# Kernel tuning notes

Hardware: AMD Instinct MI355X
Metric: run time of the kernel (lower is better)

Reference implementation:

```python
import jax, jax.numpy as jnp
import numpy as np

B, N_NODES, N_EDGES = 2, 40962, 327680
ND, ED, HD, L = 256, 64, 512, 16  # node_dim, edge_dim, hidden_dim, n_layers
LN_EPS = 1e-5


def _ln(x, g, b):
    m = jnp.mean(x, axis=-1, keepdims=True)
    v = jnp.var(x, axis=-1, keepdims=True)
    return (x - m) * jax.lax.rsqrt(v + LN_EPS) * g + b


def setup_inputs() -> dict:
    key = jax.random.key(0)
    ks = jax.random.split(key, 8)
    def w(k, shape, fan_in):
        return jax.random.normal(k, shape, jnp.float32) * (1.0 / np.sqrt(fan_in))
    node_features = jax.random.normal(ks[0], (B, N_NODES, ND), jnp.float32)
    edge_features = jax.random.normal(ks[1], (N_EDGES, ED), jnp.float32)
    edge_index = jax.random.randint(ks[2], (2, N_EDGES), 0, N_NODES, dtype=jnp.int32)
    ein, nin = ED + 2 * ND, ND + ED
    return {
        "node_features": node_features,
        "edge_features": edge_features,
        "We1": w(ks[3], (L, ein, HD), ein), "be1": jnp.zeros((L, HD), jnp.float32),
        "We2": w(ks[4], (L, HD, ED), HD),   "be2": jnp.zeros((L, ED), jnp.float32),
        "ge": jnp.ones((L, ED), jnp.float32), "ble": jnp.zeros((L, ED), jnp.float32),
        "Wn1": w(ks[5], (L, nin, HD), nin), "bn1": jnp.zeros((L, HD), jnp.float32),
        "Wn2": w(ks[6], (L, HD, ND), HD),   "bn2": jnp.zeros((L, ND), jnp.float32),
        "gn": jnp.ones((L, ND), jnp.float32), "bln": jnp.zeros((L, ND), jnp.float32),
        "edge_index": edge_index,
    }


def reference(node_features, edge_features, We1, be1, We2, be2, ge, ble,
              Wn1, bn1, Wn2, bn2, gn, bln, edge_index):
    src, dst = edge_index[0], edge_index[1]
    n = node_features.shape[-2]
    stacked = (We1, be1, We2, be2, ge, ble, Wn1, bn1, Wn2, bn2, gn, bln)

    def single(x0):  # x0: (N, ND) — original loops over batch; we vmap
        def layer(carry, p):
            x, e = carry
            we1, b1, we2, b2, g_e, b_e, wn1, nb1, wn2, nb2, g_n, b_n = p
            # edge update: gather endpoints, MLP, residual
            m = jnp.concatenate([e, x[src], x[dst]], axis=-1)   # (E, ED+2*ND)
            h = jax.nn.silu(m @ we1 + b1)                        # (E, HD)
            e = e + _ln(h @ we2 + b2, g_e, b_e)                  # (E, ED)
            # node update: scatter-sum messages to destinations, MLP, residual
            agg = jax.ops.segment_sum(e, dst, num_segments=n)    # (N, ED)
            h = jax.nn.silu(jnp.concatenate([x, agg], axis=-1) @ wn1 + nb1)
            x = x + _ln(h @ wn2 + nb2, g_n, b_n)                 # (N, ND)
            return (x, e), None
        (x, _e), _ = jax.lax.scan(layer, (x0, edge_features), stacked)
        return x

    return jax.vmap(single)(node_features)
```

## Files before the change

### kernel.cpp

```cpp
#include <hip/hip_runtime.h>
#include <hip/hip_bf16.h>

#define N_NODES 40962
#define N_EDGES 327680
#define NDIM 256
#define EDIM 64
#define HDIM 512
#define NLAYERS 16

using bf16_t = __bf16;
using bf16x4 = __bf16 __attribute__((ext_vector_type(4)));
using bf16x8 = __bf16 __attribute__((ext_vector_type(8)));
using f32x4  = float __attribute__((ext_vector_type(4)));

__device__ __forceinline__ int clamp_idx(int v) {
    return v < 0 ? 0 : (v >= N_NODES ? N_NODES - 1 : v);
}

__device__ __forceinline__ bf16x8 zero8() {
    bf16x8 z;
#pragma unroll
    for (int j = 0; j < 8; ++j) z[j] = (bf16_t)0.f;
    return z;
}

__global__ void repack_w(const float* __restrict__ src, bf16_t* __restrict__ dst,
                         int K, int N, int tilesPer) {
    int idx = blockIdx.x * 256 + threadIdx.x;
    int lane = idx & 63;
    int t = idx >> 6;
    int l = t / tilesPer;
    int tile = t % tilesPer;
    if (l >= NLAYERS) return;
    int ntN = N >> 4;
    int k0 = (tile / ntN) << 5;
    int n0 = (tile % ntN) << 4;
    int k = k0 + (lane >> 4) * 8;
    int n = n0 + (lane & 15);
    const float* s = src + (size_t)l * K * N + (size_t)k * N + n;
    bf16x8 v;
#pragma unroll
    for (int j = 0; j < 8; ++j) v[j] = (bf16_t)s[(size_t)j * N];
    *(bf16x8*)(dst + (size_t)idx * 8) = v;
}

__global__ void init_e2(const float* __restrict__ ef, bf16_t* __restrict__ es, int n8) {
    const size_t per = (size_t)N_EDGES * EDIM;
    for (int i = blockIdx.x * 256 + threadIdx.x; i < n8; i += gridDim.x * 256) {
        float4 a = *(const float4*)(ef + (size_t)i * 8);
        float4 b = *(const float4*)(ef + (size_t)i * 8 + 4);
        bf16x8 v;
        v[0] = (bf16_t)a.x; v[1] = (bf16_t)a.y; v[2] = (bf16_t)a.z; v[3] = (bf16_t)a.w;
        v[4] = (bf16_t)b.x; v[5] = (bf16_t)b.y; v[6] = (bf16_t)b.z; v[7] = (bf16_t)b.w;
        *(bf16x8*)(es + (size_t)i * 8) = v;
        *(bf16x8*)(es + per + (size_t)i * 8) = v;
    }
}

__global__ void f32_to_bf16(const float* __restrict__ src, bf16_t* __restrict__ dst, int n8) {
    for (int i = blockIdx.x * 256 + threadIdx.x; i < n8; i += gridDim.x * 256) {
        float4 a = *(const float4*)(src + (size_t)i * 8);
        float4 b = *(const float4*)(src + (size_t)i * 8 + 4);
        bf16x8 v;
        v[0] = (bf16_t)a.x; v[1] = (bf16_t)a.y; v[2] = (bf16_t)a.z; v[3] = (bf16_t)a.w;
        v[4] = (bf16_t)b.x; v[5] = (bf16_t)b.y; v[6] = (bf16_t)b.z; v[7] = (bf16_t)b.w;
        *(bf16x8*)(dst + (size_t)i * 8) = v;
    }
}

__global__ void zero_f32(float* __restrict__ p, int n4) {
    float4 z; z.x = z.y = z.z = z.w = 0.f;
    for (int i = blockIdx.x * 256 + threadIdx.x; i < n4; i += gridDim.x * 256)
        *(float4*)(p + (size_t)i * 4) = z;
}

__global__ void hist_k(const int* __restrict__ eidx, int* __restrict__ deg) {
    int e = blockIdx.x * 256 + threadIdx.x;
    if (e < N_EDGES) atomicAdd(&deg[clamp_idx(eidx[N_EDGES + e])], 1);
}

__global__ void scan_k(const int* __restrict__ deg, int* __restrict__ off,
                       int* __restrict__ cur) {
    __shared__ int part[1024];
    const int t = threadIdx.x;
    const int C = (N_NODES + 1023) / 1024;
    int lo = t * C, hi = min((t + 1) * C, N_NODES);
    int s = 0;
    for (int i = lo; i < hi; ++i) s += deg[i];
    part[t] = s;
    __syncthreads();
    for (int d = 1; d < 1024; d <<= 1) {
        int v = (t >= d) ? part[t - d] : 0;
        __syncthreads();
        part[t] += v;
        __syncthreads();
    }
    int base = (t == 0) ? 0 : part[t - 1];
    for (int i = lo; i < hi; ++i) {
        off[i] = base;
        cur[i] = base;
        base += deg[i];
    }
    if (t == 1023) off[N_NODES] = part[1023];
}

__global__ void fill_k(const int* __restrict__ eidx, int* __restrict__ cur,
                       int* __restrict__ csr) {
    int e = blockIdx.x * 256 + threadIdx.x;
    if (e < N_EDGES) {
        int d = clamp_idx(eidx[N_EDGES + e]);
        int pos = atomicAdd(&cur[d], 1);
        csr[pos] = e;
    }
}

__global__ __launch_bounds__(512, 4)
void edge_kernel(const bf16_t* __restrict__ x16, bf16_t* __restrict__ es,
                 const int* __restrict__ eidx,
                 const bf16_t* __restrict__ w1p, const float* __restrict__ b1,
                 const bf16_t* __restrict__ w2p, const float* __restrict__ b2,
                 const float* __restrict__ gw, const float* __restrict__ bw) {
    __shared__ bf16_t smem[64 * 584];
    __shared__ int sSrc[64], sDst[64];
    float* red = (float*)(smem + 64 * 520);

    const int b   = blockIdx.y;
    const int e0  = blockIdx.x * 64;
    const int tid = threadIdx.x;

    const bf16_t* xb = x16 + (size_t)b * N_NODES * NDIM;
    bf16_t* eb = es + (size_t)b * N_EDGES * EDIM;

    if (tid < 64) {
        sSrc[tid] = clamp_idx(eidx[e0 + tid]);
        sDst[tid] = clamp_idx(eidx[N_EDGES + e0 + tid]);
    }
    __syncthreads();

    {
        int r = tid >> 3, c = (tid & 7) << 3;
        *(bf16x8*)&smem[r * 584 + c] = *(const bf16x8*)(eb + (size_t)(e0 + r) * EDIM + c);
    }
#pragma unroll
    for (int k = 0; k < 4; ++k) {
        int i = tid + k * 512;
        int r = i >> 5, c = (i & 31) << 3;
        *(bf16x8*)&smem[r * 584 + 64 + c] = *(const bf16x8*)(xb + (size_t)sSrc[r] * NDIM + c);
    }
#pragma unroll
    for (int k = 0; k < 4; ++k) {
        int i = tid + k * 512;
        int r = i >> 5, c = (i & 31) << 3;
        *(bf16x8*)&smem[r * 584 + 320 + c] = *(const bf16x8*)(xb + (size_t)sDst[r] * NDIM + c);
    }
    __syncthreads();

    const int wv = tid >> 6, lane = tid & 63;
    const int m16 = lane & 15, quad = lane >> 4;

    float bias1[4];
#pragma unroll
    for (int nt = 0; nt < 4; ++nt) bias1[nt] = b1[wv * 64 + nt * 16 + m16];

    f32x4 acc1[4][4];
#pragma unroll
    for (int mt = 0; mt < 4; ++mt)
#pragma unroll
        for (int nt = 0; nt < 4; ++nt) acc1[mt][nt] = (f32x4){0.f, 0.f, 0.f, 0.f};

    const bf16x8* W1 = (const bf16x8*)w1p;
#pragma unroll 2
    for (int kc = 0; kc < 18; ++kc) {
        bf16x8 af[4];
#pragma unroll
        for (int mt = 0; mt < 4; ++mt)
            af[mt] = *(const bf16x8*)&smem[(mt * 16 + m16) * 584 + kc * 32 + quad * 8];
        bf16x8 bfr[4];
#pragma unroll
        for (int nt = 0; nt < 4; ++nt)
            bfr[nt] = W1[(size_t)(kc * 32 + wv * 4 + nt) * 64 + lane];
#pragma unroll
        for (int mt = 0; mt < 4; ++mt)
#pragma unroll
            for (int nt = 0; nt < 4; ++nt)
                acc1[mt][nt] = __builtin_amdgcn_mfma_f32_16x16x32_bf16(af[mt], bfr[nt], acc1[mt][nt], 0, 0, 0);
    }
    __syncthreads();

#pragma unroll
    for (int mt = 0; mt < 4; ++mt)
#pragma unroll
        for (int nt = 0; nt < 4; ++nt)
#pragma unroll
            for (int r = 0; r < 4; ++r) {
                int row = mt * 16 + quad * 4 + r;
                int col = wv * 64 + nt * 16 + m16;
                float v = acc1[mt][nt][r] + bias1[nt];
                v = v / (1.f + __expf(-v));
                smem[row * 520 + col] = (bf16_t)v;
            }
    __syncthreads();

    const int strip = wv >> 1, nh = wv & 1;
    f32x4 acc2[2];
#pragma unroll
    for (int nt = 0; nt < 2; ++nt) acc2[nt] = (f32x4){0.f, 0.f, 0.f, 0.f};
    const bf16x8* W2 = (const bf16x8*)w2p;
#pragma unroll 2
    for (int kc = 0; kc < 16; ++kc) {
        bf16x8 a2 = *(const bf16x8*)&smem[(strip * 16 + m16) * 520 + kc * 32 + quad * 8];
#pragma unroll
        for (int nt = 0; nt < 2; ++nt) {
            bf16x8 b2f = W2[(size_t)(kc * 4 + nh * 2 + nt) * 64 + lane];
            acc2[nt] = __builtin_amdgcn_mfma_f32_16x16x32_bf16(a2, b2f, acc2[nt], 0, 0, 0);
        }
    }

    float bias2[2], g2[2], bl2[2];
#pragma unroll
    for (int nt = 0; nt < 2; ++nt) {
        int c = nh * 32 + nt * 16 + m16;
        bias2[nt] = b2[c];
        g2[nt]    = gw[c];
        bl2[nt]   = bw[c];
    }
    float v[4][2];
#pragma unroll
    for (int r = 0; r < 4; ++r) {
        float s1 = 0.f, s2 = 0.f;
#pragma unroll
        for (int nt = 0; nt < 2; ++nt) {
            v[r][nt] = acc2[nt][r] + bias2[nt];
            s1 += v[r][nt]; s2 += v[r][nt] * v[r][nt];
        }
#pragma unroll
        for (int off = 1; off < 16; off <<= 1) {
            s1 += __shfl_xor(s1, off);
            s2 += __shfl_xor(s2, off);
        }
        if (m16 == 0) {
            int row = strip * 16 + quad * 4 + r;
            red[row * 4 + nh * 2 + 0] = s1;
            red[row * 4 + nh * 2 + 1] = s2;
        }
    }
    __syncthreads();

#pragma unroll
    for (int r = 0; r < 4; ++r) {
        int row = strip * 16 + quad * 4 + r;
        float s1 = red[row * 4 + 0] + red[row * 4 + 2];
        float s2 = red[row * 4 + 1] + red[row * 4 + 3];
        float mean = s1 * (1.f / 64.f);
        float var  = s2 * (1.f / 64.f) - mean * mean;
        float rstd = rsqrtf(fmaxf(var, 0.f) + 1e-5f);
        int eid = e0 + row;
        const bf16_t* ebr = eb + (size_t)eid * EDIM;
#pragma unroll
        for (int nt = 0; nt < 2; ++nt) {
            int c = nh * 32 + nt * 16 + m16;
            float ln = (v[r][nt] - mean) * rstd * g2[nt] + bl2[nt];
            float en = (float)ebr[c] + ln;
            smem[row * 64 + c] = (bf16_t)en;
        }
    }
    __syncthreads();
    {
        int r = tid >> 3, c = (tid & 7) << 3;
        *(bf16x8*)(eb + (size_t)(e0 + r) * EDIM + c) = *(bf16x8*)&smem[r * 64 + c];
    }
}

__global__ __launch_bounds__(512, 4)
void node_kernel(float* __restrict__ xs, bf16_t* __restrict__ x16,
                 const bf16_t* __restrict__ es,
                 const int* __restrict__ off, const int* __restrict__ csr,
                 const bf16_t* __restrict__ w1p, const float* __restrict__ b1,
                 const bf16_t* __restrict__ w2p, const float* __restrict__ b2,
                 const float* __restrict__ gw, const float* __restrict__ bw) {
    __shared__ bf16_t smem[64 * 528];
    float* red = (float*)(smem + 64 * 520);

    const int b   = blockIdx.y;
    const int n0  = blockIdx.x * 64;
    const int tid = threadIdx.x;

    float* xb = xs + (size_t)b * N_NODES * NDIM;
    bf16_t* xhb = x16 + (size_t)b * N_NODES * NDIM;
    const bf16_t* eb = es + (size_t)b * N_EDGES * EDIM;

    const int wv = tid >> 6, lane = tid & 63;
    const int m16 = lane & 15, quad = lane >> 4;

#pragma unroll
    for (int k = 0; k < 4; ++k) {
        int i = tid + k * 512;
        int r = i >> 5, c = (i & 31) << 3;
        int node = n0 + r;
        bf16x8 v = (node < N_NODES) ? *(const bf16x8*)(xhb + (size_t)node * NDIM + c)
                                    : zero8();
        *(bf16x8*)&smem[r * 328 + c] = v;
    }
#pragma unroll 1
    for (int rr = 0; rr < 8; ++rr) {
        int row = wv * 8 + rr;
        int node = n0 + row;
        float acc = 0.f;
        if (node < N_NODES) {
            int js = off[node], je = off[node + 1];
            for (int j = js; j < je; ++j) {
                int eid = csr[j];
                acc += (float)eb[(size_t)eid * EDIM + lane];
            }
        }
        smem[row * 328 + 256 + lane] = (bf16_t)acc;
    }
    __syncthreads();

    float bias1[4];
#pragma unroll
    for (int nt = 0; nt < 4; ++nt) bias1[nt] = b1[wv * 64 + nt * 16 + m16];

    f32x4 acc1[4][4];
#pragma unroll
    for (int mt = 0; mt < 4; ++mt)
#pragma unroll
        for (int nt = 0; nt < 4; ++nt) acc1[mt][nt] = (f32x4){0.f, 0.f, 0.f, 0.f};

    const bf16x8* W1 = (const bf16x8*)w1p;
#pragma unroll 2
    for (int kc = 0; kc < 10; ++kc) {
        bf16x8 af[4];
#pragma unroll
        for (int mt = 0; mt < 4; ++mt)
            af[mt] = *(const bf16x8*)&smem[(mt * 16 + m16) * 328 + kc * 32 + quad * 8];
        bf16x8 bfr[4];
#pragma unroll
        for (int nt = 0; nt < 4; ++nt)
            bfr[nt] = W1[(size_t)(kc * 32 + wv * 4 + nt) * 64 + lane];
#pragma unroll
        for (int mt = 0; mt < 4; ++mt)
#pragma unroll
            for (int nt = 0; nt < 4; ++nt)
                acc1[mt][nt] = __builtin_amdgcn_mfma_f32_16x16x32_bf16(af[mt], bfr[nt], acc1[mt][nt], 0, 0, 0);
    }
    __syncthreads();

#pragma unroll
    for (int mt = 0; mt < 4; ++mt)
#pragma unroll
        for (int nt = 0; nt < 4; ++nt)
#pragma unroll
            for (int r = 0; r < 4; ++r) {
                int row = mt * 16 + quad * 4 + r;
                int col = wv * 64 + nt * 16 + m16;
                float v = acc1[mt][nt][r] + bias1[nt];
                v = v / (1.f + __expf(-v));
                smem[row * 520 + col] = (bf16_t)v;
            }
    __syncthreads();

    const int strip = wv >> 1, nh = wv & 1;
    f32x4 acc2[8];
#pragma unroll
    for (int nt = 0; nt < 8; ++nt) acc2[nt] = (f32x4){0.f, 0.f, 0.f, 0.f};
    const bf16x8* W2 = (const bf16x8*)w2p;
#pragma unroll 2
    for (int kc = 0; kc < 16; ++kc) {
        bf16x8 a2 = *(const bf16x8*)&smem[(strip * 16 + m16) * 520 + kc * 32 + quad * 8];
#pragma unroll
        for (int nt = 0; nt < 8; ++nt) {
            bf16x8 b2f = W2[(size_t)(kc * 16 + nh * 8 + nt) * 64 + lane];
            acc2[nt] = __builtin_amdgcn_mfma_f32_16x16x32_bf16(a2, b2f, acc2[nt], 0, 0, 0);
        }
    }

    float bias2[8], g8[8], bl8[8];
#pragma unroll
    for (int nt = 0; nt < 8; ++nt) {
        int c = nh * 128 + nt * 16 + m16;
        bias2[nt] = b2[c];
        g8[nt]    = gw[c];
        bl8[nt]   = bw[c];
    }
    float v[4][8];
#pragma unroll
    for (int r = 0; r < 4; ++r) {
        float s1 = 0.f, s2 = 0.f;
#pragma unroll
        for (int nt = 0; nt < 8; ++nt) {
            v[r][nt] = acc2[nt][r] + bias2[nt];
            s1 += v[r][nt]; s2 += v[r][nt] * v[r][nt];
        }
#pragma unroll
        for (int off2 = 1; off2 < 16; off2 <<= 1) {
            s1 += __shfl_xor(s1, off2);
            s2 += __shfl_xor(s2, off2);
        }
        if (m16 == 0) {
            int row = strip * 16 + quad * 4 + r;
            red[row * 4 + nh * 2 + 0] = s1;
            red[row * 4 + nh * 2 + 1] = s2;
        }
    }
    __syncthreads();

#pragma unroll
    for (int r = 0; r < 4; ++r) {
        int row = strip * 16 + quad * 4 + r;
        int node = n0 + row;
        if (node >= N_NODES) continue;
        float s1 = red[row * 4 + 0] + red[row * 4 + 2];
        float s2 = red[row * 4 + 1] + red[row * 4 + 3];
        float mean = s1 * (1.f / 256.f);
        float var  = s2 * (1.f / 256.f) - mean * mean;
        float rstd = rsqrtf(fmaxf(var, 0.f) + 1e-5f);
#pragma unroll
        for (int nt = 0; nt < 8; ++nt) {
            int c = nh * 128 + nt * 16 + m16;
            float ln = (v[r][nt] - mean) * rstd * g8[nt] + bl8[nt];
            float* px = &xb[(size_t)node * NDIM + c];
            float nv = *px + ln;
            *px = nv;
            xhb[(size_t)node * NDIM + c] = (bf16_t)nv;
        }
    }
}

extern "C" void kernel_launch(void* const* d_in, const int* in_sizes, int n_in,
                              void* d_out, int out_size, void* d_ws, size_t ws_size,
                              hipStream_t stream) {
    const float* nf   = (const float*)d_in[0];
    const float* ef   = (const float*)d_in[1];
    const float* We1  = (const float*)d_in[2];
    const float* be1  = (const float*)d_in[3];
    const float* We2  = (const float*)d_in[4];
    const float* be2  = (const float*)d_in[5];
    const float* ge   = (const float*)d_in[6];
    const float* ble  = (const float*)d_in[7];
    const float* Wn1  = (const float*)d_in[8];
    const float* bn1  = (const float*)d_in[9];
    const float* Wn2  = (const float*)d_in[10];
    const float* bn2  = (const float*)d_in[11];
    const float* gn   = (const float*)d_in[12];
    const float* bln  = (const float*)d_in[13];
    const int* eidx   = (const int*)d_in[14];

    float* xs = (float*)d_out;

    char* p = (char*)d_ws;
    bf16_t* es  = (bf16_t*)p; p += (size_t)2 * N_EDGES * EDIM * 2;
    bf16_t* x16 = (bf16_t*)p; p += (size_t)2 * N_NODES * NDIM * 2;
    bf16_t* w1ep = (bf16_t*)p; p += (size_t)NLAYERS * 576 * 512 * 2;
    bf16_t* w2ep = (bf16_t*)p; p += (size_t)NLAYERS * 512 * 64 * 2;
    bf16_t* w1np = (bf16_t*)p; p += (size_t)NLAYERS * 320 * 512 * 2;
    bf16_t* w2np = (bf16_t*)p; p += (size_t)NLAYERS * 512 * 256 * 2;
    int* deg = (int*)p; p += (size_t)40964 * 4;
    int* off = (int*)p; p += (size_t)40964 * 4;
    int* cur = (int*)p; p += (size_t)40964 * 4;
    int* csr = (int*)p; p += (size_t)N_EDGES * 4;

    repack_w<<<2304, 256, 0, stream>>>(We1, w1ep, 576, 512, 576);
    repack_w<<<256,  256, 0, stream>>>(We2, w2ep, 512, 64,  64);
    repack_w<<<1280, 256, 0, stream>>>(Wn1, w1np, 320, 512, 320);
    repack_w<<<1024, 256, 0, stream>>>(Wn2, w2np, 512, 256, 256);

    hipMemcpyAsync(xs, nf, (size_t)out_size * 4, hipMemcpyDeviceToDevice, stream);
    f32_to_bf16<<<2048, 256, 0, stream>>>(nf, x16, 2 * N_NODES * NDIM / 8);
    init_e2<<<2048, 256, 0, stream>>>(ef, es, N_EDGES * EDIM / 8);

    zero_f32<<<64, 256, 0, stream>>>((float*)deg, 40964 / 4);
    hist_k<<<N_EDGES / 256, 256, 0, stream>>>(eidx, deg);
    scan_k<<<1, 1024, 0, stream>>>(deg, off, cur);
    fill_k<<<N_EDGES / 256, 256, 0, stream>>>(eidx, cur, csr);

    for (int l = 0; l < NLAYERS; ++l) {
        edge_kernel<<<dim3(N_EDGES / 64, 2), 512, 0, stream>>>(
            x16, es, eidx,
            w1ep + (size_t)l * 576 * 512, be1 + l * 512,
            w2ep + (size_t)l * 512 * 64,  be2 + l * 64,
            ge + l * 64, ble + l * 64);
        node_kernel<<<dim3((N_NODES + 63) / 64, 2), 512, 0, stream>>>(
            xs, x16, es, off, csr,
            w1np + (size_t)l * 320 * 512, bn1 + l * 512,
            w2np + (size_t)l * 512 * 256, bn2 + l * 256,
            gn + l * 256, bln + l * 256);
    }
}
```

Before: 12.49 ms.

## Merge both batches into one 1024-thread block sharing weight fragments

Each edge and node block now handles the same 64 edges or nodes for both batch items, 128 rows in all, with 1024 threads. Every weight fragment loaded from global memory therefore feeds twice as many MFMAs, and the src/dst indices are shared across batches. LDS rows are XOR-swizzled instead of padded, with the edge input reordered (x_src, x_dst, e) to match. Biases are folded into the accumulator init and the node gather loop is unrolled by four. The larger blocks use more LDS and registers per block and may lower occupancy, and 1024-thread blocks with launch_bounds(1024,4) may spill.

```diff
diff --git a/kernel.cpp b/kernel.cpp
--- a/kernel.cpp
+++ b/kernel.cpp
@@ -13,6 +13,9 @@
 using bf16x8 = __bf16 __attribute__((ext_vector_type(8)));
 using f32x4  = float __attribute__((ext_vector_type(4)));
 
+#define SWE(r, eo) ((r) * 576 + ((eo) ^ (((r) & 7) << 3)))
+#define SWN(r, eo) ((r) * 512 + ((eo) ^ (((r) & 7) << 3)))
+
 __device__ __forceinline__ int clamp_idx(int v) {
     return v < 0 ? 0 : (v >= N_NODES ? N_NODES - 1 : v);
 }
@@ -25,7 +28,7 @@
 }
 
 __global__ void repack_w(const float* __restrict__ src, bf16_t* __restrict__ dst,
-                         int K, int N, int tilesPer) {
+                         int K, int N, int tilesPer, int mode) {
     int idx = blockIdx.x * 256 + threadIdx.x;
     int lane = idx & 63;
     int t = idx >> 6;
@@ -37,6 +40,7 @@
     int n0 = (tile % ntN) << 4;
     int k = k0 + (lane >> 4) * 8;
     int n = n0 + (lane & 15);
+    if (mode == 1) k = (k < 512) ? k + 64 : k - 512;
     const float* s = src + (size_t)l * K * N + (size_t)k * N + n;
     bf16x8 v;
 #pragma unroll
@@ -114,22 +118,20 @@
     }
 }
 
-__global__ __launch_bounds__(512, 4)
+__global__ __launch_bounds__(1024, 4)
 void edge_kernel(const bf16_t* __restrict__ x16, bf16_t* __restrict__ es,
                  const int* __restrict__ eidx,
                  const bf16_t* __restrict__ w1p, const float* __restrict__ b1,
                  const bf16_t* __restrict__ w2p, const float* __restrict__ b2,
                  const float* __restrict__ gw, const float* __restrict__ bw) {
-    __shared__ bf16_t smem[64 * 584];
+    __shared__ bf16_t smem[128 * 576];
+    __shared__ float red[128 * 4];
     __shared__ int sSrc[64], sDst[64];
-    float* red = (float*)(smem + 64 * 520);
-
-    const int b   = blockIdx.y;
+
     const int e0  = blockIdx.x * 64;
     const int tid = threadIdx.x;
-
-    const bf16_t* xb = x16 + (size_t)b * N_NODES * NDIM;
-    bf16_t* eb = es + (size_t)b * N_EDGES * EDIM;
+    const size_t PER_E = (size_t)N_EDGES * EDIM;
+    const size_t PER_X = (size_t)N_NODES * NDIM;
 
     if (tid < 64) {
         sSrc[tid] = clamp_idx(eidx[e0 + tid]);
@@ -139,83 +141,82 @@
 
     {
         int r = tid >> 3, c = (tid & 7) << 3;
-        *(bf16x8*)&smem[r * 584 + c] = *(const bf16x8*)(eb + (size_t)(e0 + r) * EDIM + c);
+        bf16x8 v = *(const bf16x8*)(es + (size_t)(r >> 6) * PER_E
+                                       + (size_t)(e0 + (r & 63)) * EDIM + c);
+        *(bf16x8*)&smem[SWE(r, 512 + c)] = v;
     }
 #pragma unroll
     for (int k = 0; k < 4; ++k) {
-        int i = tid + k * 512;
+        int i = tid + k * 1024;
         int r = i >> 5, c = (i & 31) << 3;
-        *(bf16x8*)&smem[r * 584 + 64 + c] = *(const bf16x8*)(xb + (size_t)sSrc[r] * NDIM + c);
+        bf16x8 v = *(const bf16x8*)(x16 + (size_t)(r >> 6) * PER_X
+                                        + (size_t)sSrc[r & 63] * NDIM + c);
+        *(bf16x8*)&smem[SWE(r, c)] = v;
     }
 #pragma unroll
     for (int k = 0; k < 4; ++k) {
-        int i = tid + k * 512;
+        int i = tid + k * 1024;
         int r = i >> 5, c = (i & 31) << 3;
-        *(bf16x8*)&smem[r * 584 + 320 + c] = *(const bf16x8*)(xb + (size_t)sDst[r] * NDIM + c);
+        bf16x8 v = *(const bf16x8*)(x16 + (size_t)(r >> 6) * PER_X
+                                        + (size_t)sDst[r & 63] * NDIM + c);
+        *(bf16x8*)&smem[SWE(r, 256 + c)] = v;
     }
     __syncthreads();
 
     const int wv = tid >> 6, lane = tid & 63;
     const int m16 = lane & 15, quad = lane >> 4;
 
-    float bias1[4];
-#pragma unroll
-    for (int nt = 0; nt < 4; ++nt) bias1[nt] = b1[wv * 64 + nt * 16 + m16];
-
-    f32x4 acc1[4][4];
-#pragma unroll
-    for (int mt = 0; mt < 4; ++mt)
-#pragma unroll
-        for (int nt = 0; nt < 4; ++nt) acc1[mt][nt] = (f32x4){0.f, 0.f, 0.f, 0.f};
+    float bias1[2];
+    bias1[0] = b1[wv * 32 + m16];
+    bias1[1] = b1[wv * 32 + 16 + m16];
+
+    f32x4 acc1[8][2];
+#pragma unroll
+    for (int mt = 0; mt < 8; ++mt)
+#pragma unroll
+        for (int nt = 0; nt < 2; ++nt)
+            acc1[mt][nt] = (f32x4){bias1[nt], bias1[nt], bias1[nt], bias1[nt]};
 
     const bf16x8* W1 = (const bf16x8*)w1p;
 #pragma unroll 2
     for (int kc = 0; kc < 18; ++kc) {
-        bf16x8 af[4];
-#pragma unroll
-        for (int mt = 0; mt < 4; ++mt)
-            af[mt] = *(const bf16x8*)&smem[(mt * 16 + m16) * 584 + kc * 32 + quad * 8];
-        bf16x8 bfr[4];
-#pragma unroll
-        for (int nt = 0; nt < 4; ++nt)
-            bfr[nt] = W1[(size_t)(kc * 32 + wv * 4 + nt) * 64 + lane];
-#pragma unroll
-        for (int mt = 0; mt < 4; ++mt)
-#pragma unroll
-            for (int nt = 0; nt < 4; ++nt)
-                acc1[mt][nt] = __builtin_amdgcn_mfma_f32_16x16x32_bf16(af[mt], bfr[nt], acc1[mt][nt], 0, 0, 0);
-    }
-    __syncthreads();
-
-#pragma unroll
-    for (int mt = 0; mt < 4; ++mt)
-#pragma unroll
-        for (int nt = 0; nt < 4; ++nt)
+        bf16x8 bfr[2];
+#pragma unroll
+        for (int nt = 0; nt < 2; ++nt)
+            bfr[nt] = W1[(size_t)(kc * 32 + wv * 2 + nt) * 64 + lane];
+#pragma unroll
+        for (int g = 0; g < 2; ++g) {
+            bf16x8 af[4];
+#pragma unroll
+            for (int j = 0; j < 4; ++j) {
+                int R = g * 64 + j * 16 + m16;
+                af[j] = *(const bf16x8*)&smem[SWE(R, kc * 32 + quad * 8)];
+            }
+#pragma unroll
+            for (int j = 0; j < 4; ++j)
+#pragma unroll
+                for (int nt = 0; nt < 2; ++nt)
+                    acc1[g * 4 + j][nt] = __builtin_amdgcn_mfma_f32_16x16x32_bf16(
+                        af[j], bfr[nt], acc1[g * 4 + j][nt], 0, 0, 0);
+        }
+    }
+    __syncthreads();
+
+#pragma unroll
+    for (int mt = 0; mt < 8; ++mt)
+#pragma unroll
+        for (int nt = 0; nt < 2; ++nt)
 #pragma unroll
             for (int r = 0; r < 4; ++r) {
                 int row = mt * 16 + quad * 4 + r;
-                int col = wv * 64 + nt * 16 + m16;
-                float v = acc1[mt][nt][r] + bias1[nt];
+                int col = wv * 32 + nt * 16 + m16;
+                float v = acc1[mt][nt][r];
                 v = v / (1.f + __expf(-v));
-                smem[row * 520 + col] = (bf16_t)v;
+                smem[SWE(row, col)] = (bf16_t)v;
             }
     __syncthreads();
 
     const int strip = wv >> 1, nh = wv & 1;
-    f32x4 acc2[2];
-#pragma unroll
-    for (int nt = 0; nt < 2; ++nt) acc2[nt] = (f32x4){0.f, 0.f, 0.f, 0.f};
-    const bf16x8* W2 = (const bf16x8*)w2p;
-#pragma unroll 2
-    for (int kc = 0; kc < 16; ++kc) {
-        bf16x8 a2 = *(const bf16x8*)&smem[(strip * 16 + m16) * 520 + kc * 32 + quad * 8];
-#pragma unroll
-        for (int nt = 0; nt < 2; ++nt) {
-            bf16x8 b2f = W2[(size_t)(kc * 4 + nh * 2 + nt) * 64 + lane];
-            acc2[nt] = __builtin_amdgcn_mfma_f32_16x16x32_bf16(a2, b2f, acc2[nt], 0, 0, 0);
-        }
-    }
-
     float bias2[2], g2[2], bl2[2];
 #pragma unroll
     for (int nt = 0; nt < 2; ++nt) {
@@ -224,19 +225,35 @@
         g2[nt]    = gw[c];
         bl2[nt]   = bw[c];
     }
+    f32x4 acc2[2];
+#pragma unroll
+    for (int nt = 0; nt < 2; ++nt)
+        acc2[nt] = (f32x4){bias2[nt], bias2[nt], bias2[nt], bias2[nt]};
+    const bf16x8* W2 = (const bf16x8*)w2p;
+#pragma unroll 2
+    for (int kc = 0; kc < 16; ++kc) {
+        int R = strip * 16 + m16;
+        bf16x8 a2 = *(const bf16x8*)&smem[SWE(R, kc * 32 + quad * 8)];
+#pragma unroll
+        for (int nt = 0; nt < 2; ++nt) {
+            bf16x8 b2f = W2[(size_t)(kc * 4 + nh * 2 + nt) * 64 + lane];
+            acc2[nt] = __builtin_amdgcn_mfma_f32_16x16x32_bf16(a2, b2f, acc2[nt], 0, 0, 0);
+        }
+    }
+
     float v[4][2];
 #pragma unroll
     for (int r = 0; r < 4; ++r) {
         float s1 = 0.f, s2 = 0.f;
 #pragma unroll
         for (int nt = 0; nt < 2; ++nt) {
-            v[r][nt] = acc2[nt][r] + bias2[nt];
+            v[r][nt] = acc2[nt][r];
             s1 += v[r][nt]; s2 += v[r][nt] * v[r][nt];
         }
 #pragma unroll
-        for (int off = 1; off < 16; off <<= 1) {
-            s1 += __shfl_xor(s1, off);
-            s2 += __shfl_xor(s2, off);
+        for (int o = 1; o < 16; o <<= 1) {
+            s1 += __shfl_xor(s1, o);
+            s2 += __shfl_xor(s2, o);
         }
         if (m16 == 0) {
             int row = strip * 16 + quad * 4 + r;
@@ -246,6 +263,7 @@
     }
     __syncthreads();
 
+    float en[4][2];
 #pragma unroll
     for (int r = 0; r < 4; ++r) {
         int row = strip * 16 + quad * 4 + r;
@@ -254,127 +272,135 @@
         float mean = s1 * (1.f / 64.f);
         float var  = s2 * (1.f / 64.f) - mean * mean;
         float rstd = rsqrtf(fmaxf(var, 0.f) + 1e-5f);
-        int eid = e0 + row;
-        const bf16_t* ebr = eb + (size_t)eid * EDIM;
 #pragma unroll
         for (int nt = 0; nt < 2; ++nt) {
             int c = nh * 32 + nt * 16 + m16;
             float ln = (v[r][nt] - mean) * rstd * g2[nt] + bl2[nt];
-            float en = (float)ebr[c] + ln;
-            smem[row * 64 + c] = (bf16_t)en;
+            en[r][nt] = (float)smem[SWE(row, 512 + c)] + ln;
+        }
+    }
+    __syncthreads();
+
+#pragma unroll
+    for (int r = 0; r < 4; ++r) {
+        int row = strip * 16 + quad * 4 + r;
+#pragma unroll
+        for (int nt = 0; nt < 2; ++nt) {
+            int c = nh * 32 + nt * 16 + m16;
+            smem[row * 64 + c] = (bf16_t)en[r][nt];
         }
     }
     __syncthreads();
     {
         int r = tid >> 3, c = (tid & 7) << 3;
-        *(bf16x8*)(eb + (size_t)(e0 + r) * EDIM + c) = *(bf16x8*)&smem[r * 64 + c];
-    }
-}
-
-__global__ __launch_bounds__(512, 4)
+        *(bf16x8*)(es + (size_t)(r >> 6) * PER_E + (size_t)(e0 + (r & 63)) * EDIM + c) =
+            *(bf16x8*)&smem[r * 64 + c];
+    }
+}
+
+__global__ __launch_bounds__(1024, 4)
 void node_kernel(float* __restrict__ xs, bf16_t* __restrict__ x16,
                  const bf16_t* __restrict__ es,
                  const int* __restrict__ off, const int* __restrict__ csr,
                  const bf16_t* __restrict__ w1p, const float* __restrict__ b1,
                  const bf16_t* __restrict__ w2p, const float* __restrict__ b2,
                  const float* __restrict__ gw, const float* __restrict__ bw) {
-    __shared__ bf16_t smem[64 * 528];
-    float* red = (float*)(smem + 64 * 520);
-
-    const int b   = blockIdx.y;
+    __shared__ bf16_t smem[128 * 512];
+    __shared__ float red[128 * 4];
+
     const int n0  = blockIdx.x * 64;
     const int tid = threadIdx.x;
-
-    float* xb = xs + (size_t)b * N_NODES * NDIM;
-    bf16_t* xhb = x16 + (size_t)b * N_NODES * NDIM;
-    const bf16_t* eb = es + (size_t)b * N_EDGES * EDIM;
+    const size_t PER_E = (size_t)N_EDGES * EDIM;
+    const size_t PER_X = (size_t)N_NODES * NDIM;
 
     const int wv = tid >> 6, lane = tid & 63;
     const int m16 = lane & 15, quad = lane >> 4;
 
 #pragma unroll
     for (int k = 0; k < 4; ++k) {
-        int i = tid + k * 512;
+        int i = tid + k * 1024;
         int r = i >> 5, c = (i & 31) << 3;
-        int node = n0 + r;
-        bf16x8 v = (node < N_NODES) ? *(const bf16x8*)(xhb + (size_t)node * NDIM + c)
-                                    : zero8();
-        *(bf16x8*)&smem[r * 328 + c] = v;
+        int node = n0 + (r & 63);
+        bf16x8 v = (node < N_NODES)
+            ? *(const bf16x8*)(x16 + (size_t)(r >> 6) * PER_X + (size_t)node * NDIM + c)
+            : zero8();
+        *(bf16x8*)&smem[SWN(r, c)] = v;
     }
 #pragma unroll 1
     for (int rr = 0; rr < 8; ++rr) {
         int row = wv * 8 + rr;
-        int node = n0 + row;
+        int node = n0 + (row & 63);
         float acc = 0.f;
         if (node < N_NODES) {
+            const bf16_t* ebb = es + (size_t)(row >> 6) * PER_E;
             int js = off[node], je = off[node + 1];
-            for (int j = js; j < je; ++j) {
-                int eid = csr[j];
-                acc += (float)eb[(size_t)eid * EDIM + lane];
+            int j = js;
+            for (; j + 4 <= je; j += 4) {
+                int i0 = csr[j], i1 = csr[j + 1], i2 = csr[j + 2], i3 = csr[j + 3];
+                float a0 = (float)ebb[(size_t)i0 * EDIM + lane];
+                float a1 = (float)ebb[(size_t)i1 * EDIM + lane];
+                float a2 = (float)ebb[(size_t)i2 * EDIM + lane];
+                float a3 = (float)ebb[(size_t)i3 * EDIM + lane];
+                acc += (a0 + a1) + (a2 + a3);
             }
-        }
-        smem[row * 328 + 256 + lane] = (bf16_t)acc;
-    }
-    __syncthreads();
-
-    float bias1[4];
-#pragma unroll
-    for (int nt = 0; nt < 4; ++nt) bias1[nt] = b1[wv * 64 + nt * 16 + m16];
-
-    f32x4 acc1[4][4];
-#pragma unroll
-    for (int mt = 0; mt < 4; ++mt)
-#pragma unroll
-        for (int nt = 0; nt < 4; ++nt) acc1[mt][nt] = (f32x4){0.f, 0.f, 0.f, 0.f};
+            for (; j < je; ++j)
+                acc += (float)ebb[(size_t)csr[j] * EDIM + lane];
+        }
+        smem[SWN(row, 256 + lane)] = (bf16_t)acc;
+    }
+    __syncthreads();
+
+    float bias1[2];
+    bias1[0] = b1[wv * 32 + m16];
+    bias1[1] = b1[wv * 32 + 16 + m16];
+
+    f32x4 acc1[8][2];
+#pragma unroll
+    for (int mt = 0; mt < 8; ++mt)
+#pragma unroll
+        for (int nt = 0; nt < 2; ++nt)
+            acc1[mt][nt] = (f32x4){bias1[nt], bias1[nt], bias1[nt], bias1[nt]};
 
     const bf16x8* W1 = (const bf16x8*)w1p;
 #pragma unroll 2
     for (int kc = 0; kc < 10; ++kc) {
-        bf16x8 af[4];
-#pragma unroll
-        for (int mt = 0; mt < 4; ++mt)
-            af[mt] = *(const bf16x8*)&smem[(mt * 16 + m16) * 328 + kc * 32 + quad * 8];
-        bf16x8 bfr[4];
-#pragma unroll
-        for (int nt = 0; nt < 4; ++nt)
-            bfr[nt] = W1[(size_t)(kc * 32 + wv * 4 + nt) * 64 + lane];
-#pragma unroll
-        for (int mt = 0; mt < 4; ++mt)
-#pragma unroll
-            for (int nt = 0; nt < 4; ++nt)
-                acc1[mt][nt] = __builtin_amdgcn_mfma_f32_16x16x32_bf16(af[mt], bfr[nt], acc1[mt][nt], 0, 0, 0);
-    }
-    __syncthreads();
-
-#pragma unroll
-    for (int mt = 0; mt < 4; ++mt)
-#pragma unroll
-        for (int nt = 0; nt < 4; ++nt)
+        bf16x8 bfr[2];
+#pragma unroll
+        for (int nt = 0; nt < 2; ++nt)
+            bfr[nt] = W1[(size_t)(kc * 32 + wv * 2 + nt) * 64 + lane];
+#pragma unroll
+        for (int g = 0; g < 2; ++g) {
+            bf16x8 af[4];
+#pragma unroll
+            for (int j = 0; j < 4; ++j) {
+                int R = g * 64 + j * 16 + m16;
+                af[j] = *(const bf16x8*)&smem[SWN(R, kc * 32 + quad * 8)];
+            }
+#pragma unroll
+            for (int j = 0; j < 4; ++j)
+#pragma unroll
+                for (int nt = 0; nt < 2; ++nt)
+                    acc1[g * 4 + j][nt] = __builtin_amdgcn_mfma_f32_16x16x32_bf16(
+                        af[j], bfr[nt], acc1[g * 4 + j][nt], 0, 0, 0);
+        }
+    }
+    __syncthreads();
+
+#pragma unroll
+    for (int mt = 0; mt < 8; ++mt)
+#pragma unroll
+        for (int nt = 0; nt < 2; ++nt)
 #pragma unroll
             for (int r = 0; r < 4; ++r) {
                 int row = mt * 16 + quad * 4 + r;
-                int col = wv * 64 + nt * 16 + m16;
-                float v = acc1[mt][nt][r] + bias1[nt];
+                int col = wv * 32 + nt * 16 + m16;
+                float v = acc1[mt][nt][r];
                 v = v / (1.f + __expf(-v));
-                smem[row * 520 + col] = (bf16_t)v;
+                smem[SWN(row, col)] = (bf16_t)v;
             }
     __syncthreads();
 
     const int strip = wv >> 1, nh = wv & 1;
-    f32x4 acc2[8];
-#pragma unroll
-    for (int nt = 0; nt < 8; ++nt) acc2[nt] = (f32x4){0.f, 0.f, 0.f, 0.f};
-    const bf16x8* W2 = (const bf16x8*)w2p;
-#pragma unroll 2
-    for (int kc = 0; kc < 16; ++kc) {
-        bf16x8 a2 = *(const bf16x8*)&smem[(strip * 16 + m16) * 520 + kc * 32 + quad * 8];
-#pragma unroll
-        for (int nt = 0; nt < 8; ++nt) {
-            bf16x8 b2f = W2[(size_t)(kc * 16 + nh * 8 + nt) * 64 + lane];
-            acc2[nt] = __builtin_amdgcn_mfma_f32_16x16x32_bf16(a2, b2f, acc2[nt], 0, 0, 0);
-        }
-    }
-
     float bias2[8], g8[8], bl8[8];
 #pragma unroll
     for (int nt = 0; nt < 8; ++nt) {
@@ -383,19 +409,35 @@
         g8[nt]    = gw[c];
         bl8[nt]   = bw[c];
     }
+    f32x4 acc2[8];
+#pragma unroll
+    for (int nt = 0; nt < 8; ++nt)
+        acc2[nt] = (f32x4){bias2[nt], bias2[nt], bias2[nt], bias2[nt]};
+    const bf16x8* W2 = (const bf16x8*)w2p;
+#pragma unroll 2
+    for (int kc = 0; kc < 16; ++kc) {
+        int R = strip * 16 + m16;
+        bf16x8 a2 = *(const bf16x8*)&smem[SWN(R, kc * 32 + quad * 8)];
+#pragma unroll
+        for (int nt = 0; nt < 8; ++nt) {
+            bf16x8 b2f = W2[(size_t)(kc * 16 + nh * 8 + nt) * 64 + lane];
+            acc2[nt] = __builtin_amdgcn_mfma_f32_16x16x32_bf16(a2, b2f, acc2[nt], 0, 0, 0);
+        }
+    }
+
     float v[4][8];
 #pragma unroll
     for (int r = 0; r < 4; ++r) {
         float s1 = 0.f, s2 = 0.f;
 #pragma unroll
         for (int nt = 0; nt < 8; ++nt) {
-            v[r][nt] = acc2[nt][r] + bias2[nt];
+            v[r][nt] = acc2[nt][r];
             s1 += v[r][nt]; s2 += v[r][nt] * v[r][nt];
         }
 #pragma unroll
-        for (int off2 = 1; off2 < 16; off2 <<= 1) {
-            s1 += __shfl_xor(s1, off2);
-            s2 += __shfl_xor(s2, off2);
+        for (int o = 1; o < 16; o <<= 1) {
+            s1 += __shfl_xor(s1, o);
+            s2 += __shfl_xor(s2, o);
         }
         if (m16 == 0) {
             int row = strip * 16 + quad * 4 + r;
@@ -408,21 +450,23 @@
 #pragma unroll
     for (int r = 0; r < 4; ++r) {
         int row = strip * 16 + quad * 4 + r;
-        int node = n0 + row;
+        int node = n0 + (row & 63);
         if (node >= N_NODES) continue;
+        int batch = row >> 6;
         float s1 = red[row * 4 + 0] + red[row * 4 + 2];
         float s2 = red[row * 4 + 1] + red[row * 4 + 3];
         float mean = s1 * (1.f / 256.f);
         float var  = s2 * (1.f / 256.f) - mean * mean;
         float rstd = rsqrtf(fmaxf(var, 0.f) + 1e-5f);
+        float* xb = xs + (size_t)batch * PER_X + (size_t)node * NDIM;
+        bf16_t* xhb = x16 + (size_t)batch * PER_X + (size_t)node * NDIM;
 #pragma unroll
         for (int nt = 0; nt < 8; ++nt) {
             int c = nh * 128 + nt * 16 + m16;
             float ln = (v[r][nt] - mean) * rstd * g8[nt] + bl8[nt];
-            float* px = &xb[(size_t)node * NDIM + c];
-            float nv = *px + ln;
-            *px = nv;
-            xhb[(size_t)node * NDIM + c] = (bf16_t)nv;
+            float nv = xb[c] + ln;
+            xb[c] = nv;
+            xhb[c] = (bf16_t)nv;
         }
     }
 }
@@ -460,10 +504,10 @@
     int* cur = (int*)p; p += (size_t)40964 * 4;
     int* csr = (int*)p; p += (size_t)N_EDGES * 4;
 
-    repack_w<<<2304, 256, 0, stream>>>(We1, w1ep, 576, 512, 576);
-    repack_w<<<256,  256, 0, stream>>>(We2, w2ep, 512, 64,  64);
-    repack_w<<<1280, 256, 0, stream>>>(Wn1, w1np, 320, 512, 320);
-    repack_w<<<1024, 256, 0, stream>>>(Wn2, w2np, 512, 256, 256);
+    repack_w<<<2304, 256, 0, stream>>>(We1, w1ep, 576, 512, 576, 1);
+    repack_w<<<256,  256, 0, stream>>>(We2, w2ep, 512, 64,  64,  0);
+    repack_w<<<1280, 256, 0, stream>>>(Wn1, w1np, 320, 512, 320, 0);
+    repack_w<<<1024, 256, 0, stream>>>(Wn2, w2np, 512, 256, 256, 0);
 
     hipMemcpyAsync(xs, nf, (size_t)out_size * 4, hipMemcpyDeviceToDevice, stream);
     f32_to_bf16<<<2048, 256, 0, stream>>>(nf, x16, 2 * N_NODES * NDIM / 8);
@@ -475,12 +519,12 @@
     fill_k<<<N_EDGES / 256, 256, 0, stream>>>(eidx, cur, csr);
 
     for (int l = 0; l < NLAYERS; ++l) {
-        edge_kernel<<<dim3(N_EDGES / 64, 2), 512, 0, stream>>>(
+        edge_kernel<<<dim3(N_EDGES / 64), 1024, 0, stream>>>(
             x16, es, eidx,
             w1ep + (size_t)l * 576 * 512, be1 + l * 512,
             w2ep + (size_t)l * 512 * 64,  be2 + l * 64,
             ge + l * 64, ble + l * 64);
-        node_kernel<<<dim3((N_NODES + 63) / 64, 2), 512, 0, stream>>>(
+        node_kernel<<<dim3((N_NODES + 63) / 64), 1024, 0, stream>>>(
             xs, x16, es, off, csr,
             w1np + (size_t)l * 320 * 512, bn1 + l * 512,
             w2np + (size_t)l * 512 * 256, bn2 + l * 256,
```

New measurement: 13.75 ms. +10.1%, slower.
